# Performance work log

Measured on AMD Instinct MI355X. Metric: run time of the kernel, lower is better.

Reference implementation:

```python
import jax, jax.numpy as jnp
import numpy as np

B, F = 1024, 784
OUT, OR_T, AND_T = 1024, 32, 16
IDX_RANGE = 1 + 2 * F  # column 0 is the constant-true column


def setup_inputs() -> dict:
    key = jax.random.key(0)
    kx, kw = jax.random.split(key)
    # Binary inputs (0/1) stored as float32; module calls x.bool() i.e. x != 0.
    x = jax.random.randint(kx, (B, F), 0, 2).astype(jnp.float32)
    # Integer gate wiring: indices into [const_true | x | ~x].
    weights = jax.random.randint(kw, (OUT, OR_T, AND_T), 0, IDX_RANGE).astype(jnp.int32)
    return {"x": x, "weights": weights}


def reference(x, weights):
    out_f, or_t, and_t = weights.shape
    b = x.shape[0]
    xb = x != 0                                            # [B, F] bool
    ones = jnp.ones((b, 1), dtype=bool)
    x_in = jnp.concatenate([ones, xb, ~xb], axis=1)        # [B, 1+2F]
    # or_padding_mask: an OR-term is active unless all its AND indices are 0
    or_mask = ~jnp.all(weights == 0, axis=-1)              # [OUT, OR_T]
    # Gather selected booleans, then AND over and_terms, OR over or_terms
    x_sel = x_in[:, weights.reshape(-1)]                   # [B, OUT*OR_T*AND_T]
    x_bin = x_sel.reshape(b, out_f, or_t, and_t)
    x_and = jnp.all(x_bin, axis=-1) & or_mask              # [B, OUT, OR_T]
    x_or = jnp.any(x_and, axis=-1)                         # [B, OUT]
    return x_or
```

## Files before the change

kernel.cpp:

```cpp
#include <hip/hip_runtime.h>
#include <stdint.h>

#define BATCH 1024
#define FEAT  784
#define OUTF  1024
#define OR_T  32
#define AND_T 16
#define NIDX  1569
#define TKDIM 512
#define TK2   256
#define WROW  65

typedef unsigned long long u64;

__global__ __launch_bounds__(1024) void fused2(const float* __restrict__ x,
                                               const int* __restrict__ w,
                                               int* __restrict__ out) {
    __shared__ u64 lbits[1600];
    __shared__ unsigned int widx[TK2 * WROW];
    __shared__ u64 red[1024];

    const int bid  = blockIdx.x;
    const int xcd  = bid & 7;
    const int s    = bid >> 3;
    const int g    = xcd * 2 + (s & 1);
    const int ob   = s >> 1;
    const int tid  = threadIdx.x;
    const int lane = tid & 63;
    const int wv   = tid >> 6;

    const int4* wsrc = (const int4*)(w + (size_t)ob * 64 * TKDIM);
    #pragma unroll
    for (int t = 0; t < 8; ++t) {
        const int q4 = t * 1024 + tid;
        const int4 v = wsrc[q4];
        const int o  = q4 >> 7;
        const int tk = (q4 & 127) * 4;
        const int r  = tk >> 1;
        widx[(r + 0) * WROW + o] =
            ((unsigned int)v.x & 0xFFFFu) | ((unsigned int)v.y << 16);
        widx[(r + 1) * WROW + o] =
            ((unsigned int)v.z & 0xFFFFu) | ((unsigned int)v.w << 16);
    }

    const int start = wv * 12 + (wv < 4 ? wv : 4);
    const int cnt   = (wv < 4) ? 13 : 12;
    const float4* xrow = (const float4*)(x + (size_t)(g * 64 + lane) * FEAT);
    for (int i = 0; i < cnt; ++i) {
        const int f4 = start + i;
        const float4 v = xrow[f4];
        const int f = f4 * 4;
        const u64 m0 = __ballot(v.x != 0.0f);
        const u64 m1 = __ballot(v.y != 0.0f);
        const u64 m2 = __ballot(v.z != 0.0f);
        const u64 m3 = __ballot(v.w != 0.0f);
        const u64 mv = (lane == 0) ? m0 : (lane == 1) ? m1 : (lane == 2) ? m2 : m3;
        if (lane < 4) {
            lbits[1 + f + lane]   = mv;
            lbits[785 + f + lane] = ~mv;
        }
    }
    if (tid == 0) lbits[0] = ~0ull;
    __syncthreads();

    const int o_local = lane;
    const int tg      = wv;

    u64 orv = 0;
    #pragma unroll
    for (int tt = 0; tt < 2; ++tt) {
        const int term = tg * 2 + tt;
        const unsigned int* wrow = widx + (term * 8) * WROW + o_local;
        u64 a = ~0ull;
        unsigned int zor = 0;
        #pragma unroll
        for (int kk = 0; kk < 8; ++kk) {
            const unsigned int pk = wrow[kk * WROW];
            zor |= pk;
            a &= lbits[pk & 0xFFFFu];
            a &= lbits[pk >> 16];
        }
        if (zor != 0) orv |= a;
    }

    red[tid] = orv;
    __syncthreads();

    u64 full = 0;
    #pragma unroll
    for (int j = 0; j < 16; ++j) full |= red[o_local + j * 64];

    int* outg = out + (size_t)(g * 64) * OUTF + (size_t)ob * 64;
    #pragma unroll
    for (int jj = 0; jj < 4; ++jj) {
        const int j = tg * 4 + jj;
        outg[(size_t)j * OUTF + o_local] = (int)((full >> j) & 1);
    }
}

extern "C" void kernel_launch(void* const* d_in, const int* in_sizes, int n_in,
                              void* d_out, int out_size, void* d_ws, size_t ws_size,
                              hipStream_t stream) {
    (void)in_sizes; (void)n_in; (void)d_ws; (void)ws_size;
    const float* x = (const float*)d_in[0];
    const int*   w = (const int*)d_in[1];
    int* out = (int*)d_out;

    fused2<<<256, 1024, 0, stream>>>(x, w, out);
}
```

Measured before the change: 75.12 us.

## Stage x bit-packing through a double-buffered coalesced shared tile

Replaces the per-lane row-strided float4 loads of x, where each lane read a different row, with coalesced loads in which 16 threads cover 64 contiguous floats of a row. Each float4 is reduced to a nibble in a double-buffered shared tile, and wavefronts then ballot from the tile to build the lbits bitmasks. The intent is better global load coalescing and overlapping the next chunk's load with the current chunk's ballots. In exchange it adds 13 block-wide __syncthreads iterations, which may cost more than the coalescing saves.

```diff
diff --git a/kernel.cpp b/kernel.cpp
--- a/kernel.cpp
+++ b/kernel.cpp
@@ -10,15 +10,17 @@
 #define TKDIM 512
 #define TK2   256
 #define WROW  65
+#define TROW  17
 
 typedef unsigned long long u64;
 
-__global__ __launch_bounds__(1024) void fused2(const float* __restrict__ x,
+__global__ __launch_bounds__(1024) void fused3(const float* __restrict__ x,
                                                const int* __restrict__ w,
                                                int* __restrict__ out) {
     __shared__ u64 lbits[1600];
     __shared__ unsigned int widx[TK2 * WROW];
     __shared__ u64 red[1024];
+    __shared__ unsigned int tile[2][64 * TROW];
 
     const int bid  = blockIdx.x;
     const int xcd  = bid & 7;
@@ -29,39 +31,70 @@
     const int lane = tid & 63;
     const int wv   = tid >> 6;
 
+    const float* xg = x + (size_t)(g * 64) * FEAT;
+
+    {
+        const int r = tid >> 4;
+        const int q = tid & 15;
+        const float4 v = *(const float4*)(xg + (size_t)r * FEAT + q * 4);
+        const unsigned int nib = (v.x != 0.0f ? 1u : 0u)
+                               | (v.y != 0.0f ? 2u : 0u)
+                               | (v.z != 0.0f ? 4u : 0u)
+                               | (v.w != 0.0f ? 8u : 0u);
+        tile[0][r * TROW + q] = nib;
+    }
+
     const int4* wsrc = (const int4*)(w + (size_t)ob * 64 * TKDIM);
     #pragma unroll
     for (int t = 0; t < 8; ++t) {
         const int q4 = t * 1024 + tid;
         const int4 v = wsrc[q4];
         const int o  = q4 >> 7;
-        const int tk = (q4 & 127) * 4;
-        const int r  = tk >> 1;
-        widx[(r + 0) * WROW + o] =
+        const int rr = (q4 & 127) * 2;
+        widx[(rr + 0) * WROW + o] =
             ((unsigned int)v.x & 0xFFFFu) | ((unsigned int)v.y << 16);
-        widx[(r + 1) * WROW + o] =
+        widx[(rr + 1) * WROW + o] =
             ((unsigned int)v.z & 0xFFFFu) | ((unsigned int)v.w << 16);
-    }
-
-    const int start = wv * 12 + (wv < 4 ? wv : 4);
-    const int cnt   = (wv < 4) ? 13 : 12;
-    const float4* xrow = (const float4*)(x + (size_t)(g * 64 + lane) * FEAT);
-    for (int i = 0; i < cnt; ++i) {
-        const int f4 = start + i;
-        const float4 v = xrow[f4];
-        const int f = f4 * 4;
-        const u64 m0 = __ballot(v.x != 0.0f);
-        const u64 m1 = __ballot(v.y != 0.0f);
-        const u64 m2 = __ballot(v.z != 0.0f);
-        const u64 m3 = __ballot(v.w != 0.0f);
-        const u64 mv = (lane == 0) ? m0 : (lane == 1) ? m1 : (lane == 2) ? m2 : m3;
-        if (lane < 4) {
-            lbits[1 + f + lane]   = mv;
-            lbits[785 + f + lane] = ~mv;
-        }
     }
     if (tid == 0) lbits[0] = ~0ull;
     __syncthreads();
+
+    for (int i = 0; i < 13; ++i) {
+        unsigned int nib = 0;
+        int r = 0, q = 0;
+        bool st = false;
+        if (i < 12) {
+            const int ii = i + 1;
+            if (ii < 12) {
+                r = tid >> 4; q = tid & 15; st = true;
+                const float4 v = *(const float4*)(xg + (size_t)r * FEAT
+                                                  + ii * 64 + q * 4);
+                nib = (v.x != 0.0f ? 1u : 0u) | (v.y != 0.0f ? 2u : 0u)
+                    | (v.z != 0.0f ? 4u : 0u) | (v.w != 0.0f ? 8u : 0u);
+            } else if (tid < 256) {
+                r = tid >> 2; q = tid & 3; st = true;
+                const float4 v = *(const float4*)(xg + (size_t)r * FEAT
+                                                  + 768 + q * 4);
+                nib = (v.x != 0.0f ? 1u : 0u) | (v.y != 0.0f ? 2u : 0u)
+                    | (v.z != 0.0f ? 4u : 0u) | (v.w != 0.0f ? 8u : 0u);
+            }
+        }
+
+        const int nq = (i < 12) ? 16 : 4;
+        if (wv < nq) {
+            const unsigned int vr = tile[i & 1][lane * TROW + wv];
+            #pragma unroll
+            for (int j = 0; j < 4; ++j) {
+                const u64 m = __ballot(((vr >> j) & 1u) != 0u);
+                const int f = i * 64 + wv * 4 + j;
+                if (lane < 2)
+                    lbits[(lane ? 785 : 1) + f] = lane ? ~m : m;
+            }
+        }
+
+        if (st) tile[(i + 1) & 1][r * TROW + q] = nib;
+        __syncthreads();
+    }
 
     const int o_local = lane;
     const int tg      = wv;
@@ -106,5 +139,5 @@
     const int*   w = (const int*)d_in[1];
     int* out = (int*)d_out;
 
-    fused2<<<256, 1024, 0, stream>>>(x, w, out);
+    fused3<<<256, 1024, 0, stream>>>(x, w, out);
 }
```

Result: faster. 70.37 us (-6.3%).

## Split input bit-packing across grid via cooperative launch and global workspace

Applied to the files above, without the earlier changes.

Replaces the 256-block kernel, in which every block re-packs its batch group's input bits, with a 1024-block, 256-thread cooperative kernel. In the new kernel each block packs a slice of x into a global bitset workspace once, then a grid-wide sync follows and each block copies its group's bits into shared memory. Each block now handles 16 outputs instead of 64, so the grid is larger and occupancy is finer-grained. The cost is a grid-wide barrier and a global round-trip for the bitsets, which adds latency on a kernel that is already short. A fallback non-cooperative kernel is kept for when the workspace is too small.

```diff
diff --git a/kernel.cpp b/kernel.cpp
--- a/kernel.cpp
+++ b/kernel.cpp
@@ -1,4 +1,5 @@
 #include <hip/hip_runtime.h>
+#include <hip/hip_cooperative_groups.h>
 #include <stdint.h>
 
 #define BATCH 1024
@@ -7,41 +8,127 @@
 #define OR_T  32
 #define AND_T 16
 #define NIDX  1569
-#define TKDIM 512
-#define TK2   256
-#define WROW  65
+#define BSTRIDE 1600
+#define NGROUP  16
+#define TKDIM   512
+#define WPAD    257
+
+#define WS_NEED ((size_t)NGROUP * BSTRIDE * 8)
 
 typedef unsigned long long u64;
-
-__global__ __launch_bounds__(1024) void fused2(const float* __restrict__ x,
-                                               const int* __restrict__ w,
-                                               int* __restrict__ out) {
-    __shared__ u64 lbits[1600];
-    __shared__ unsigned int widx[TK2 * WROW];
-    __shared__ u64 red[1024];
+typedef __attribute__((ext_vector_type(2))) u64 u64x2;
+
+namespace cg = cooperative_groups;
+
+__global__ __launch_bounds__(256) void fusedc(const float* __restrict__ x,
+                                              const int* __restrict__ w,
+                                              u64* __restrict__ bits,
+                                              int* __restrict__ out) {
+    __shared__ __align__(16) u64 lbits[BSTRIDE];
+    __shared__ unsigned int widx[16 * WPAD];
+    __shared__ u64 red[256];
 
     const int bid  = blockIdx.x;
-    const int xcd  = bid & 7;
-    const int s    = bid >> 3;
-    const int g    = xcd * 2 + (s & 1);
-    const int ob   = s >> 1;
     const int tid  = threadIdx.x;
     const int lane = tid & 63;
     const int wv   = tid >> 6;
 
-    const int4* wsrc = (const int4*)(w + (size_t)ob * 64 * TKDIM);
+    const int xcd = bid & 7;
+    const int s   = bid >> 3;
+    const int ob  = xcd + 8 * (s & 1);
+    const int q   = (s >> 1) & 3;
+    const int g   = s >> 3;
+
+    const int4* wsrc = (const int4*)(w + (size_t)(ob * 64 + q * 16) * TKDIM);
     #pragma unroll
     for (int t = 0; t < 8; ++t) {
-        const int q4 = t * 1024 + tid;
+        const int q4 = t * 256 + tid;
         const int4 v = wsrc[q4];
         const int o  = q4 >> 7;
-        const int tk = (q4 & 127) * 4;
-        const int r  = tk >> 1;
-        widx[(r + 0) * WROW + o] =
+        const int r  = (q4 & 127) * 2;
+        widx[o * WPAD + r] =
             ((unsigned int)v.x & 0xFFFFu) | ((unsigned int)v.y << 16);
-        widx[(r + 1) * WROW + o] =
+        widx[o * WPAD + r + 1] =
             ((unsigned int)v.z & 0xFFFFu) | ((unsigned int)v.w << 16);
     }
+
+    const int u = wv * 1024 + bid;
+    if (u < 3136) {
+        const int pg = u / 196;
+        const int f4 = u % 196;
+        const float4 v = *(const float4*)(x + (size_t)(pg * 64 + lane) * FEAT
+                                            + f4 * 4);
+        u64* bg = bits + (size_t)pg * BSTRIDE;
+        const u64 m0 = __ballot(v.x != 0.0f);
+        const u64 m1 = __ballot(v.y != 0.0f);
+        const u64 m2 = __ballot(v.z != 0.0f);
+        const u64 m3 = __ballot(v.w != 0.0f);
+        const u64 mv = (lane == 0) ? m0 : (lane == 1) ? m1 : (lane == 2) ? m2 : m3;
+        const int f = f4 * 4;
+        if (lane < 4) {
+            bg[1 + f + lane]   = mv;
+            bg[785 + f + lane] = ~mv;
+        }
+        if (f4 == 0 && lane == 4) bg[0] = ~0ull;
+    }
+
+    __threadfence();
+    cg::this_grid().sync();
+
+    const u64* bg2 = bits + (size_t)g * BSTRIDE;
+    #pragma unroll
+    for (int i = 0; i < 4; ++i) {
+        const int t = i * 256 + tid;
+        if (t < BSTRIDE / 2) ((u64x2*)lbits)[t] = ((const u64x2*)bg2)[t];
+    }
+    __syncthreads();
+
+    const int ol = tid & 15;
+    const int tg = tid >> 4;
+
+    u64 orv = 0;
+    #pragma unroll
+    for (int tt = 0; tt < 2; ++tt) {
+        const int term = tg * 2 + tt;
+        const unsigned int* wr = widx + ol * WPAD + term * 8;
+        u64 a = ~0ull;
+        unsigned int zor = 0;
+        #pragma unroll
+        for (int kk = 0; kk < 8; ++kk) {
+            const unsigned int pk = wr[kk];
+            zor |= pk;
+            a &= lbits[pk & 0xFFFFu];
+            a &= lbits[pk >> 16];
+        }
+        if (zor != 0) orv |= a;
+    }
+
+    red[tid] = orv;
+    __syncthreads();
+
+    u64 full = 0;
+    #pragma unroll
+    for (int j = 0; j < 16; ++j) full |= red[j * 16 + ol];
+
+    int* outg = out + (size_t)(g * 64) * OUTF + (size_t)ob * 64 + q * 16;
+    #pragma unroll
+    for (int jj = 0; jj < 4; ++jj) {
+        const int j = tg * 4 + jj;
+        outg[(size_t)j * OUTF + ol] = (int)((full >> j) & 1);
+    }
+}
+
+__global__ __launch_bounds__(1024) void binlayer_fused(const float* __restrict__ x,
+                                                       const int* __restrict__ w,
+                                                       int* __restrict__ out) {
+    __shared__ u64 lbits[BSTRIDE];
+    __shared__ u64 red[1024];
+
+    const int g    = blockIdx.x;
+    const int ob   = blockIdx.y;
+    const int tid  = threadIdx.x;
+    const int lane = tid & 63;
+    const int wv   = tid >> 6;
 
     const int start = wv * 12 + (wv < 4 ? wv : 4);
     const int cnt   = (wv < 4) ? 13 : 12;
@@ -63,22 +150,24 @@
     if (tid == 0) lbits[0] = ~0ull;
     __syncthreads();
 
-    const int o_local = lane;
-    const int tg      = wv;
+    const int o_local = tid & 63;
+    const int tg      = tid >> 6;
+    const int o       = ob * 64 + o_local;
+    const int4* wq = (const int4*)(w + ((size_t)o * OR_T + tg * 2) * AND_T);
 
     u64 orv = 0;
     #pragma unroll
     for (int tt = 0; tt < 2; ++tt) {
-        const int term = tg * 2 + tt;
-        const unsigned int* wrow = widx + (term * 8) * WROW + o_local;
         u64 a = ~0ull;
-        unsigned int zor = 0;
+        int zor = 0;
         #pragma unroll
-        for (int kk = 0; kk < 8; ++kk) {
-            const unsigned int pk = wrow[kk * WROW];
-            zor |= pk;
-            a &= lbits[pk & 0xFFFFu];
-            a &= lbits[pk >> 16];
+        for (int k = 0; k < 4; ++k) {
+            const int4 wi = wq[tt * 4 + k];
+            zor |= wi.x | wi.y | wi.z | wi.w;
+            a &= lbits[wi.x];
+            a &= lbits[wi.y];
+            a &= lbits[wi.z];
+            a &= lbits[wi.w];
         }
         if (zor != 0) orv |= a;
     }
@@ -101,10 +190,17 @@
 extern "C" void kernel_launch(void* const* d_in, const int* in_sizes, int n_in,
                               void* d_out, int out_size, void* d_ws, size_t ws_size,
                               hipStream_t stream) {
-    (void)in_sizes; (void)n_in; (void)d_ws; (void)ws_size;
+    (void)in_sizes; (void)n_in;
     const float* x = (const float*)d_in[0];
     const int*   w = (const int*)d_in[1];
     int* out = (int*)d_out;
 
-    fused2<<<256, 1024, 0, stream>>>(x, w, out);
+    if (ws_size >= WS_NEED) {
+        u64* bits = (u64*)d_ws;
+        void* args[] = {(void*)&x, (void*)&w, (void*)&bits, (void*)&out};
+        hipLaunchCooperativeKernel((const void*)fusedc, dim3(1024), dim3(256),
+                                   args, 0, stream);
+    } else {
+        binlayer_fused<<<dim3(NGROUP, OUTF / 64), 1024, 0, stream>>>(x, w, out);
+    }
 }
```

After: 237.6 us. 3.16x slower.

## Coalesce x staging via shared nibble buffer and halve output tile per block

Applied to the files above, without the earlier changes.

The kernel now launches 512 blocks of 512 threads, each handling 32 outputs instead of 64. The input rows are first loaded with coalesced float4 reads and packed into per-row 4-bit nibbles in shared memory. Ballots then build the batch bitmasks from that buffer, replacing the old strided per-lane row reads from global memory. The weight index table is stored output-major with padding so each thread reads consecutive entries. The trade-off is that each x tile is reloaded by twice as many blocks, and the extra staging pass adds a barrier.

```diff
diff --git a/kernel.cpp b/kernel.cpp
--- a/kernel.cpp
+++ b/kernel.cpp
@@ -7,75 +7,93 @@
 #define OR_T  32
 #define AND_T 16
 #define NIDX  1569
-#define TKDIM 512
-#define TK2   256
-#define WROW  65
+#define NGROUP  16
+#define TKDIM   512
+#define WPAD    257
+#define NIBROW  204
 
 typedef unsigned long long u64;
 
-__global__ __launch_bounds__(1024) void fused2(const float* __restrict__ x,
-                                               const int* __restrict__ w,
-                                               int* __restrict__ out) {
+__global__ __launch_bounds__(512) void fused5(const float* __restrict__ x,
+                                              const int* __restrict__ w,
+                                              int* __restrict__ out) {
     __shared__ u64 lbits[1600];
-    __shared__ unsigned int widx[TK2 * WROW];
-    __shared__ u64 red[1024];
+    __shared__ unsigned int widx[32 * WPAD];
+    __shared__ unsigned char nib[64 * NIBROW];
+    __shared__ u64 red[512];
 
     const int bid  = blockIdx.x;
     const int xcd  = bid & 7;
     const int s    = bid >> 3;
     const int g    = xcd * 2 + (s & 1);
-    const int ob   = s >> 1;
+    const int obh  = s >> 1;
     const int tid  = threadIdx.x;
     const int lane = tid & 63;
     const int wv   = tid >> 6;
 
-    const int4* wsrc = (const int4*)(w + (size_t)ob * 64 * TKDIM);
+    const float* xg = x + (size_t)(g * 64) * FEAT;
+    #pragma unroll
+    for (int i = 0; i < 25; ++i) {
+        const int idx = i * 512 + tid;
+        if (idx < 12544) {
+            const int r = idx / 196;
+            const int c = idx - r * 196;
+            const float4 v = *(const float4*)(xg + (size_t)r * FEAT + c * 4);
+            nib[r * NIBROW + c] = (unsigned char)((v.x != 0.0f ? 1u : 0u)
+                                                | (v.y != 0.0f ? 2u : 0u)
+                                                | (v.z != 0.0f ? 4u : 0u)
+                                                | (v.w != 0.0f ? 8u : 0u));
+        }
+    }
+
+    const int4* wsrc = (const int4*)(w + (size_t)(obh * 32) * TKDIM);
     #pragma unroll
     for (int t = 0; t < 8; ++t) {
-        const int q4 = t * 1024 + tid;
+        const int q4 = t * 512 + tid;
         const int4 v = wsrc[q4];
         const int o  = q4 >> 7;
-        const int tk = (q4 & 127) * 4;
-        const int r  = tk >> 1;
-        widx[(r + 0) * WROW + o] =
+        const int r  = (q4 & 127) * 2;
+        widx[o * WPAD + r] =
             ((unsigned int)v.x & 0xFFFFu) | ((unsigned int)v.y << 16);
-        widx[(r + 1) * WROW + o] =
+        widx[o * WPAD + r + 1] =
             ((unsigned int)v.z & 0xFFFFu) | ((unsigned int)v.w << 16);
     }
+    __syncthreads();
 
-    const int start = wv * 12 + (wv < 4 ? wv : 4);
-    const int cnt   = (wv < 4) ? 13 : 12;
-    const float4* xrow = (const float4*)(x + (size_t)(g * 64 + lane) * FEAT);
-    for (int i = 0; i < cnt; ++i) {
-        const int f4 = start + i;
-        const float4 v = xrow[f4];
-        const int f = f4 * 4;
-        const u64 m0 = __ballot(v.x != 0.0f);
-        const u64 m1 = __ballot(v.y != 0.0f);
-        const u64 m2 = __ballot(v.z != 0.0f);
-        const u64 m3 = __ballot(v.w != 0.0f);
-        const u64 mv = (lane == 0) ? m0 : (lane == 1) ? m1 : (lane == 2) ? m2 : m3;
-        if (lane < 4) {
-            lbits[1 + f + lane]   = mv;
-            lbits[785 + f + lane] = ~mv;
+    #pragma unroll
+    for (int i = 0; i < 25; ++i) {
+        const int c = i * 8 + wv;
+        if (c < 196) {
+            const unsigned int nv = nib[lane * NIBROW + c];
+            const u64 m0 = __ballot((nv & 1u) != 0u);
+            const u64 m1 = __ballot((nv & 2u) != 0u);
+            const u64 m2 = __ballot((nv & 4u) != 0u);
+            const u64 m3 = __ballot((nv & 8u) != 0u);
+            const u64 mv = (lane == 0) ? m0 : (lane == 1) ? m1
+                         : (lane == 2) ? m2 : m3;
+            const int f = c * 4;
+            if (lane < 4) {
+                lbits[1 + f + lane]   = mv;
+                lbits[785 + f + lane] = ~mv;
+            }
         }
     }
     if (tid == 0) lbits[0] = ~0ull;
     __syncthreads();
 
-    const int o_local = lane;
-    const int tg      = wv;
+    const int ol = tid & 31;
+    const int tg = tid >> 5;
 
     u64 orv = 0;
     #pragma unroll
     for (int tt = 0; tt < 2; ++tt) {
         const int term = tg * 2 + tt;
-        const unsigned int* wrow = widx + (term * 8) * WROW + o_local;
+        const unsigned int* wr = widx + ol * WPAD + term * 8;
         u64 a = ~0ull;
         unsigned int zor = 0;
         #pragma unroll
         for (int kk = 0; kk < 8; ++kk) {
-            const unsigned int pk = wrow[kk * WROW];
+            const unsigned int pk = wr[kk];
             zor |= pk;
             a &= lbits[pk & 0xFFFFu];
             a &= lbits[pk >> 16];
@@ -88,13 +106,13 @@
 
     u64 full = 0;
     #pragma unroll
-    for (int j = 0; j < 16; ++j) full |= red[o_local + j * 64];
+    for (int j = 0; j < 16; ++j) full |= red[j * 32 + ol];
 
-    int* outg = out + (size_t)(g * 64) * OUTF + (size_t)ob * 64;
+    int* outg = out + (size_t)(g * 64) * OUTF + (size_t)obh * 32;
     #pragma unroll
     for (int jj = 0; jj < 4; ++jj) {
         const int j = tg * 4 + jj;
-        outg[(size_t)j * OUTF + o_local] = (int)((full >> j) & 1);
+        outg[(size_t)j * OUTF + ol] = (int)((full >> j) & 1);
     }
 }
 
@@ -106,5 +124,5 @@
     const int*   w = (const int*)d_in[1];
     int* out = (int*)d_out;
 
-    fused2<<<256, 1024, 0, stream>>>(x, w, out);
+    fused5<<<512, 512, 0, stream>>>(x, w, out);
 }
```

After: 70.96 us. 5.5% less time.
